# Kernel optimization log

Hardware: AMD Instinct MI355X
Metric: run time of the kernel (lower is better)

The kernel has to match this reference:

```python
import jax, jax.numpy as jnp
import numpy as np

D_MODEL = 1024
H = 16
D_K = D_MODEL // H  # 64
RANK = 5
ALPHA = 1.0


def _lora_linear(x, W, b, dW, dB):
    # merged weight: W + alpha * dB @ dW  (shape [out, in]); F.linear -> x @ W_merged.T + b
    Wm = W + ALPHA * (dB @ dW)
    return x @ Wm.T + b


def setup_inputs() -> dict:
    key = jax.random.key(0)
    ks = jax.random.split(key, 16)
    b_s, nq = 2, 2048
    s = 1.0 / np.sqrt(D_MODEL).astype(np.float32)
    inp = {
        "x": jax.random.normal(ks[0], (b_s, nq, D_MODEL), dtype=jnp.float32),
    }
    names = ["q", "k", "v", "o"]
    i = 1
    for n in names:
        inp[f"{n}_w"] = jax.random.normal(ks[i], (D_MODEL, D_MODEL), dtype=jnp.float32) * s; i += 1
        inp[f"{n}_b"] = jnp.zeros((D_MODEL,), dtype=jnp.float32)
        inp[f"{n}_dw"] = jax.random.normal(ks[i], (RANK, D_MODEL), dtype=jnp.float32) * 0.01; i += 1
        inp[f"{n}_db"] = jax.random.normal(ks[i], (D_MODEL, RANK), dtype=jnp.float32) * 0.01; i += 1
    return inp


def reference(x, q_w, q_b, q_dw, q_db, k_w, k_b, k_dw, k_db,
              v_w, v_b, v_dw, v_db, o_w, o_b, o_dw, o_db):
    b_s, nq, _ = x.shape
    q = _lora_linear(x, q_w, q_b, q_dw, q_db).reshape(b_s, nq, H, D_K)
    k = _lora_linear(x, k_w, k_b, k_dw, k_db).reshape(b_s, nq, H, D_K)
    v = _lora_linear(x, v_w, v_b, v_dw, v_db).reshape(b_s, nq, H, D_K)
    # scores: [b, h, q, k]
    att = jnp.einsum("bqhd,bkhd->bhqk", q, k) / np.sqrt(D_K).astype(np.float32)
    att = jax.nn.softmax(att, axis=-1)
    out = jnp.einsum("bhqk,bkhd->bqhd", att, v).reshape(b_s, nq, H * D_K)
    out = _lora_linear(out, o_w, o_b, o_dw, o_db)
    return out
```

## Files before the change

### kernel.cpp

```cpp
#include <hip/hip_runtime.h>
#include <hip/hip_bf16.h>

#define NQ 2048
#define NB 2

typedef unsigned short u16;
typedef unsigned int u32;
typedef _Float16 f16;
typedef __attribute__((ext_vector_type(8))) _Float16 half8;
typedef __attribute__((ext_vector_type(2))) __fp16 fp16x2;
typedef __attribute__((ext_vector_type(4))) float f32x4;

#define MFMAH(A, B, C) __builtin_amdgcn_mfma_f32_16x16x32_f16(A, B, C, 0, 0, 0)

__device__ __forceinline__ u16 f2h(float x) {
    f16 h = (f16)x;
    return *(u16*)&h;
}
__device__ __forceinline__ u32 pk_h2(float a, float b) {
    union { fp16x2 v; u32 u; } c;
    c.v = __builtin_amdgcn_cvt_pkrtz(a, b);
    return c.u;
}
__device__ __forceinline__ void glds16(const u16* g, u16* l) {
    typedef const __attribute__((address_space(1))) u16 gu16;
    typedef __attribute__((address_space(3))) u16 lu16;
    __builtin_amdgcn_global_load_lds((gu16*)g, (lu16*)l, 16, 0, 0);
}

__global__ __launch_bounds__(256) void merge_w16(
    const float* __restrict__ w0, const float* __restrict__ dw0, const float* __restrict__ db0,
    const float* __restrict__ w1, const float* __restrict__ dw1, const float* __restrict__ db1,
    const float* __restrict__ w2, const float* __restrict__ dw2, const float* __restrict__ db2,
    const float* __restrict__ w3, const float* __restrict__ dw3, const float* __restrict__ db3,
    u16* __restrict__ Wf) {
    int idx = blockIdx.x * 256 + threadIdx.x;
    int row = idx >> 10, col = idx & 1023;
    int which = row >> 10, lr = row & 1023;
    const float* W  = (which == 0) ? w0  : (which == 1) ? w1  : (which == 2) ? w2  : w3;
    const float* dW = (which == 0) ? dw0 : (which == 1) ? dw1 : (which == 2) ? dw2 : dw3;
    const float* dB = (which == 0) ? db0 : (which == 1) ? db1 : (which == 2) ? db2 : db3;
    float acc = W[lr * 1024 + col];
#pragma unroll
    for (int r = 0; r < 5; ++r) acc += dB[lr * 5 + r] * dW[r * 1024 + col];
    if (which == 0) acc *= 0.125f;
    Wf[idx] = f2h(acc);
}

__global__ __launch_bounds__(256) void bias_pack(
    const float* __restrict__ b0, const float* __restrict__ b1,
    const float* __restrict__ b2, const float* __restrict__ b3,
    float* __restrict__ ball) {
    int t = blockIdx.x * 256 + threadIdx.x;
    int which = t >> 10;
    const float* B = (which == 0) ? b0 : (which == 1) ? b1 : (which == 2) ? b2 : b3;
    float v = B[t & 1023];
    if (which == 0) v *= 0.125f;
    ball[t] = v;
}

__global__ __launch_bounds__(256) void xcast(const float* __restrict__ x,
                                             u16* __restrict__ xf) {
    int i4 = (blockIdx.x * 256 + threadIdx.x) * 4;
    float4 v = *(const float4*)&x[i4];
    *(uint2*)&xf[i4] = make_uint2(pk_h2(v.x, v.y), pk_h2(v.z, v.w));
}

template <int TM>
__global__ __launch_bounds__(256) void gemm_f16(
    const u16* __restrict__ Af, const u16* __restrict__ Bf,
    const float* __restrict__ bias,
    float* __restrict__ Cf, u16* __restrict__ Cb, int ldc,
    u16* __restrict__ VtOut) {
    constexpr int MI = TM / 32;
    __shared__ u16 As[2][TM * 32];
    __shared__ u16 Bs[2][128 * 32];
    const int tid = threadIdx.x;
    const int wid = tid >> 6, lane = tid & 63;
    const int ln = lane & 15, quad = lane >> 4;
    const int bm = blockIdx.y * TM, bn = blockIdx.x * 128;
    const int wm = (wid >> 1) * (TM / 2), wn = (wid & 1) * 64;
    const int lrow = lane >> 2;
    const int lchunk = (lane & 3) * 8;

    f32x4 acc[MI][4];
#pragma unroll
    for (int i = 0; i < MI; ++i)
#pragma unroll
        for (int j = 0; j < 4; ++j) acc[i][j] = (f32x4){0.f, 0.f, 0.f, 0.f};

    for (int k0 = 0; k0 < 1024; k0 += 64) {
#pragma unroll
        for (int hf = 0; hf < 2; ++hf) {
#pragma unroll
            for (int p = 0; p < TM / 64; ++p) {
                int r = p * 64 + wid * 16;
                glds16(&Af[(bm + r + lrow) * 1024 + k0 + hf * 32 + lchunk],
                       &As[hf][r * 32]);
            }
#pragma unroll
            for (int p = 0; p < 2; ++p) {
                int r = p * 64 + wid * 16;
                glds16(&Bf[(bn + r + lrow) * 1024 + k0 + hf * 32 + lchunk],
                       &Bs[hf][r * 32]);
            }
        }
        asm volatile("s_waitcnt vmcnt(0)" ::: "memory");
        __syncthreads();

        half8 a[MI][2], b[4][2];
#pragma unroll
        for (int kc = 0; kc < 2; ++kc) {
#pragma unroll
            for (int j = 0; j < 4; ++j)
                b[j][kc] = *(const half8*)&Bs[kc][(wn + j * 16 + ln) * 32 + quad * 8];
#pragma unroll
            for (int i = 0; i < MI; ++i)
                a[i][kc] = *(const half8*)&As[kc][(wm + i * 16 + ln) * 32 + quad * 8];
        }
#pragma unroll
        for (int i = 0; i < MI; ++i)
#pragma unroll
            for (int j = 0; j < 4; ++j) {
                acc[i][j] = MFMAH(a[i][0], b[j][0], acc[i][j]);
                acc[i][j] = MFMAH(a[i][1], b[j][1], acc[i][j]);
            }
        __syncthreads();
    }

    if (VtOut && bn >= 2048) {
#pragma unroll
        for (int i = 0; i < MI; ++i)
#pragma unroll
            for (int j = 0; j < 4; ++j) {
                int col = bn + wn + j * 16 + ln;
                float bv = bias[col];
                int colV = col - 2048;
                int row0 = bm + wm + i * 16 + quad * 4;
                ushort4 pk = make_ushort4(f2h(acc[i][j][0] + bv), f2h(acc[i][j][1] + bv),
                                          f2h(acc[i][j][2] + bv), f2h(acc[i][j][3] + bv));
                *(ushort4*)&VtOut[colV * 4096 + row0] = pk;
            }
        return;
    }

#pragma unroll
    for (int i = 0; i < MI; ++i)
#pragma unroll
        for (int j = 0; j < 4; ++j) {
            int col = bn + wn + j * 16 + ln;
            float bv = bias[col];
#pragma unroll
            for (int r = 0; r < 4; ++r) {
                int row = bm + wm + i * 16 + quad * 4 + r;
                float v = acc[i][j][r] + bv;
                if (Cb) Cb[row * ldc + col] = f2h(v);
                else    Cf[row * ldc + col] = v;
            }
        }
}

__global__ __launch_bounds__(256) void flash_f16(
    const u16* __restrict__ QKV, const u16* __restrict__ Vt,
    u16* __restrict__ AO) {
    __shared__ u16 Ks[2][64 * 72];
    __shared__ u16 Vs[2][64 * 72];
    __shared__ u16 Ps[4][32 * 72];

    const int tid = threadIdx.x;
    const int wid = tid >> 6, lane = tid & 63;
    const int ln = lane & 15, quad = lane >> 4;
    const int qt = blockIdx.x, h = blockIdx.y, b = blockIdx.z;
    const int rowbase = b * NQ;
    const int col0 = h * 64;
    const int q0 = rowbase + qt * 128 + wid * 32;

    const half8 ones = {(f16)1, (f16)1, (f16)1, (f16)1,
                        (f16)1, (f16)1, (f16)1, (f16)1};

    half8 qf[2][2];
#pragma unroll
    for (int mi = 0; mi < 2; ++mi)
#pragma unroll
        for (int kc = 0; kc < 2; ++kc)
            qf[mi][kc] = *(const half8*)&QKV[(q0 + mi * 16 + ln) * 3072 + col0 +
                                             kc * 32 + quad * 8];

    f32x4 accO[4][2];
    f32x4 accS[2];
#pragma unroll
    for (int mi = 0; mi < 2; ++mi) {
        accS[mi] = (f32x4){0.f, 0.f, 0.f, 0.f};
#pragma unroll
        for (int a = 0; a < 4; ++a) accO[a][mi] = (f32x4){0.f, 0.f, 0.f, 0.f};
    }

    const int srow = tid >> 2;
    const int sc0 = (tid & 3) * 16;
    const int NT = NQ / 64;

    {
        const u16* kg = QKV + (rowbase + srow) * 3072 + 1024 + col0;
        const u16* vg = Vt + (col0 + srow) * 4096 + rowbase;
        *(uint4*)&Ks[0][srow * 72 + sc0]     = *(const uint4*)&kg[sc0];
        *(uint4*)&Ks[0][srow * 72 + sc0 + 8] = *(const uint4*)&kg[sc0 + 8];
        *(uint4*)&Vs[0][srow * 72 + sc0]     = *(const uint4*)&vg[sc0];
        *(uint4*)&Vs[0][srow * 72 + sc0 + 8] = *(const uint4*)&vg[sc0 + 8];
    }
    __syncthreads();

    for (int kt = 0; kt < NT; ++kt) {
        const int cur = kt & 1;
        uint4 nk0, nk1, nv0, nv1;
        if (kt + 1 < NT) {
            const u16* kg = QKV + (rowbase + (kt + 1) * 64 + srow) * 3072 + 1024 + col0;
            const u16* vg = Vt + (col0 + srow) * 4096 + rowbase + (kt + 1) * 64;
            nk0 = *(const uint4*)&kg[sc0];
            nk1 = *(const uint4*)&kg[sc0 + 8];
            nv0 = *(const uint4*)&vg[sc0];
            nv1 = *(const uint4*)&vg[sc0 + 8];
        }

        f32x4 s[4][2];
#pragma unroll
        for (int a = 0; a < 4; ++a) {
            half8 kf0 = *(const half8*)&Ks[cur][(a * 16 + ln) * 72 + quad * 8];
            half8 kf1 = *(const half8*)&Ks[cur][(a * 16 + ln) * 72 + 32 + quad * 8];
#pragma unroll
            for (int mi = 0; mi < 2; ++mi) {
                f32x4 t = (f32x4){0.f, 0.f, 0.f, 0.f};
                t = MFMAH(kf0, qf[mi][0], t);
                t = MFMAH(kf1, qf[mi][1], t);
                s[a][mi] = t;
            }
        }

#pragma unroll
        for (int mi = 0; mi < 2; ++mi)
#pragma unroll
            for (int a = 0; a < 4; ++a) {
                float p0 = __expf(s[a][mi][0]), p1 = __expf(s[a][mi][1]);
                float p2 = __expf(s[a][mi][2]), p3 = __expf(s[a][mi][3]);
                uint2 w = make_uint2(pk_h2(p0, p1), pk_h2(p2, p3));
                *(uint2*)&Ps[wid][(mi * 16 + ln) * 72 + a * 16 + quad * 4] = w;
            }

        asm volatile("s_waitcnt lgkmcnt(0)" ::: "memory");

        half8 pf[2][2];
#pragma unroll
        for (int mi = 0; mi < 2; ++mi)
#pragma unroll
            for (int kc = 0; kc < 2; ++kc) {
                pf[mi][kc] = *(const half8*)&Ps[wid][(mi * 16 + ln) * 72 +
                                                     kc * 32 + quad * 8];
                accS[mi] = MFMAH(ones, pf[mi][kc], accS[mi]);
            }

#pragma unroll
        for (int a = 0; a < 4; ++a) {
            half8 vf0 = *(const half8*)&Vs[cur][(a * 16 + ln) * 72 + quad * 8];
            half8 vf1 = *(const half8*)&Vs[cur][(a * 16 + ln) * 72 + 32 + quad * 8];
#pragma unroll
            for (int mi = 0; mi < 2; ++mi) {
                accO[a][mi] = MFMAH(vf0, pf[mi][0], accO[a][mi]);
                accO[a][mi] = MFMAH(vf1, pf[mi][1], accO[a][mi]);
            }
        }

        if (kt + 1 < NT) {
            const int nb = cur ^ 1;
            *(uint4*)&Ks[nb][srow * 72 + sc0]     = nk0;
            *(uint4*)&Ks[nb][srow * 72 + sc0 + 8] = nk1;
            *(uint4*)&Vs[nb][srow * 72 + sc0]     = nv0;
            *(uint4*)&Vs[nb][srow * 72 + sc0 + 8] = nv1;
        }
        __syncthreads();
    }

#pragma unroll
    for (int mi = 0; mi < 2; ++mi) {
        float inv = 1.f / accS[mi][0];
        int q = q0 + mi * 16 + ln;
#pragma unroll
        for (int a = 0; a < 4; ++a) {
            ushort4 pk = make_ushort4(f2h(accO[a][mi][0] * inv),
                                      f2h(accO[a][mi][1] * inv),
                                      f2h(accO[a][mi][2] * inv),
                                      f2h(accO[a][mi][3] * inv));
            *(ushort4*)&AO[q * 1024 + col0 + a * 16 + quad * 4] = pk;
        }
    }
}

extern "C" void kernel_launch(void* const* d_in, const int* in_sizes, int n_in,
                              void* d_out, int out_size, void* d_ws, size_t ws_size,
                              hipStream_t stream) {
    const float* x = (const float*)d_in[0];
    const float* w[4]  = {(const float*)d_in[1],  (const float*)d_in[5],
                          (const float*)d_in[9],  (const float*)d_in[13]};
    const float* bv[4] = {(const float*)d_in[2],  (const float*)d_in[6],
                          (const float*)d_in[10], (const float*)d_in[14]};
    const float* dw[4] = {(const float*)d_in[3],  (const float*)d_in[7],
                          (const float*)d_in[11], (const float*)d_in[15]};
    const float* db[4] = {(const float*)d_in[4],  (const float*)d_in[8],
                          (const float*)d_in[12], (const float*)d_in[16]};

    u16* p = (u16*)d_ws;
    u16* Wf  = p; p += 4096 * 1024;
    u16* xf  = p; p += 4096 * 1024;
    u16* QKV = p; p += 4096 * 3072;
    u16* Vt  = p; p += 1024 * 4096;
    float* ball = (float*)p;
    u16* AO = xf;

    merge_w16<<<16384, 256, 0, stream>>>(w[0], dw[0], db[0], w[1], dw[1], db[1],
                                         w[2], dw[2], db[2], w[3], dw[3], db[3], Wf);
    bias_pack<<<16, 256, 0, stream>>>(bv[0], bv[1], bv[2], bv[3], ball);
    xcast<<<4096, 256, 0, stream>>>(x, xf);

    gemm_f16<128><<<dim3(24, 32), 256, 0, stream>>>(xf, Wf, ball,
                                                    nullptr, QKV, 3072, Vt);

    flash_f16<<<dim3(NQ / 128, 16, NB), 256, 0, stream>>>(QKV, Vt, AO);

    gemm_f16<64><<<dim3(8, 64), 256, 0, stream>>>(AO, Wf + 3072 * 1024,
                                                  ball + 3072, (float*)d_out, nullptr, 1024,
                                                  nullptr);
}
```

Measured before the change: 237.1 us.

## Use direct global-to-LDS loads for K/V tiles and fold log2e into Q scale

The K and V tile staging in the flash kernel now uses global_load_lds to copy straight into shared memory, replacing the register round-trip. The smem layout changes from padded 72-stride rows to unpadded 32-wide halves, which may add bank conflicts on fragment reads. Separately, the Q scale now includes log2(e), so the softmax can use the hardware exp2 instead of __expf, saving a multiply per element.

```diff
diff --git a/kernel.cpp b/kernel.cpp
--- a/kernel.cpp
+++ b/kernel.cpp
@@ -22,11 +22,20 @@
     c.v = __builtin_amdgcn_cvt_pkrtz(a, b);
     return c.u;
 }
+__device__ __forceinline__ float fexp2(float x) {
+#if __has_builtin(__builtin_amdgcn_exp2f)
+    return __builtin_amdgcn_exp2f(x);
+#else
+    return exp2f(x);
+#endif
+}
 __device__ __forceinline__ void glds16(const u16* g, u16* l) {
     typedef const __attribute__((address_space(1))) u16 gu16;
     typedef __attribute__((address_space(3))) u16 lu16;
     __builtin_amdgcn_global_load_lds((gu16*)g, (lu16*)l, 16, 0, 0);
 }
+
+#define QSCALE 0.18033688011112042f
 
 __global__ __launch_bounds__(256) void merge_w16(
     const float* __restrict__ w0, const float* __restrict__ dw0, const float* __restrict__ db0,
@@ -43,7 +52,7 @@
     float acc = W[lr * 1024 + col];
 #pragma unroll
     for (int r = 0; r < 5; ++r) acc += dB[lr * 5 + r] * dW[r * 1024 + col];
-    if (which == 0) acc *= 0.125f;
+    if (which == 0) acc *= QSCALE;
     Wf[idx] = f2h(acc);
 }
 
@@ -55,7 +64,7 @@
     int which = t >> 10;
     const float* B = (which == 0) ? b0 : (which == 1) ? b1 : (which == 2) ? b2 : b3;
     float v = B[t & 1023];
-    if (which == 0) v *= 0.125f;
+    if (which == 0) v *= QSCALE;
     ball[t] = v;
 }
 
@@ -163,8 +172,8 @@
 __global__ __launch_bounds__(256) void flash_f16(
     const u16* __restrict__ QKV, const u16* __restrict__ Vt,
     u16* __restrict__ AO) {
-    __shared__ u16 Ks[2][64 * 72];
-    __shared__ u16 Vs[2][64 * 72];
+    __shared__ u16 Ks[2][2][64 * 32];
+    __shared__ u16 Vs[2][2][64 * 32];
     __shared__ u16 Ps[4][32 * 72];
 
     const int tid = threadIdx.x;
@@ -174,6 +183,8 @@
     const int rowbase = b * NQ;
     const int col0 = h * 64;
     const int q0 = rowbase + qt * 128 + wid * 32;
+    const int drow = lane >> 2;
+    const int dchunk = (lane & 3) * 8;
 
     const half8 ones = {(f16)1, (f16)1, (f16)1, (f16)1,
                         (f16)1, (f16)1, (f16)1, (f16)1};
@@ -195,37 +206,35 @@
         for (int a = 0; a < 4; ++a) accO[a][mi] = (f32x4){0.f, 0.f, 0.f, 0.f};
     }
 
-    const int srow = tid >> 2;
-    const int sc0 = (tid & 3) * 16;
     const int NT = NQ / 64;
 
-    {
-        const u16* kg = QKV + (rowbase + srow) * 3072 + 1024 + col0;
-        const u16* vg = Vt + (col0 + srow) * 4096 + rowbase;
-        *(uint4*)&Ks[0][srow * 72 + sc0]     = *(const uint4*)&kg[sc0];
-        *(uint4*)&Ks[0][srow * 72 + sc0 + 8] = *(const uint4*)&kg[sc0 + 8];
-        *(uint4*)&Vs[0][srow * 72 + sc0]     = *(const uint4*)&vg[sc0];
-        *(uint4*)&Vs[0][srow * 72 + sc0 + 8] = *(const uint4*)&vg[sc0 + 8];
-    }
+#define STAGE(buf, kt)                                                                 \
+    {                                                                                  \
+        int ktbase = rowbase + (kt) * 64;                                              \
+        _Pragma("unroll")                                                              \
+        for (int hf = 0; hf < 2; ++hf)                                                 \
+            glds16(&QKV[(ktbase + wid * 16 + drow) * 3072 + 1024 + col0 + hf * 32 +    \
+                        dchunk],                                                       \
+                   &Ks[buf][hf][wid * 16 * 32]);                                       \
+        _Pragma("unroll")                                                              \
+        for (int kh = 0; kh < 2; ++kh)                                                 \
+            glds16(&Vt[(col0 + wid * 16 + drow) * 4096 + ktbase + kh * 32 + dchunk],   \
+                   &Vs[buf][kh][wid * 16 * 32]);                                       \
+    }
+
+    STAGE(0, 0)
+    asm volatile("s_waitcnt vmcnt(0)" ::: "memory");
     __syncthreads();
 
     for (int kt = 0; kt < NT; ++kt) {
         const int cur = kt & 1;
-        uint4 nk0, nk1, nv0, nv1;
-        if (kt + 1 < NT) {
-            const u16* kg = QKV + (rowbase + (kt + 1) * 64 + srow) * 3072 + 1024 + col0;
-            const u16* vg = Vt + (col0 + srow) * 4096 + rowbase + (kt + 1) * 64;
-            nk0 = *(const uint4*)&kg[sc0];
-            nk1 = *(const uint4*)&kg[sc0 + 8];
-            nv0 = *(const uint4*)&vg[sc0];
-            nv1 = *(const uint4*)&vg[sc0 + 8];
-        }
+        if (kt + 1 < NT) STAGE(cur ^ 1, kt + 1)
 
         f32x4 s[4][2];
 #pragma unroll
         for (int a = 0; a < 4; ++a) {
-            half8 kf0 = *(const half8*)&Ks[cur][(a * 16 + ln) * 72 + quad * 8];
-            half8 kf1 = *(const half8*)&Ks[cur][(a * 16 + ln) * 72 + 32 + quad * 8];
+            half8 kf0 = *(const half8*)&Ks[cur][0][(a * 16 + ln) * 32 + quad * 8];
+            half8 kf1 = *(const half8*)&Ks[cur][1][(a * 16 + ln) * 32 + quad * 8];
 #pragma unroll
             for (int mi = 0; mi < 2; ++mi) {
                 f32x4 t = (f32x4){0.f, 0.f, 0.f, 0.f};
@@ -239,8 +248,8 @@
         for (int mi = 0; mi < 2; ++mi)
 #pragma unroll
             for (int a = 0; a < 4; ++a) {
-                float p0 = __expf(s[a][mi][0]), p1 = __expf(s[a][mi][1]);
-                float p2 = __expf(s[a][mi][2]), p3 = __expf(s[a][mi][3]);
+                float p0 = fexp2(s[a][mi][0]), p1 = fexp2(s[a][mi][1]);
+                float p2 = fexp2(s[a][mi][2]), p3 = fexp2(s[a][mi][3]);
                 uint2 w = make_uint2(pk_h2(p0, p1), pk_h2(p2, p3));
                 *(uint2*)&Ps[wid][(mi * 16 + ln) * 72 + a * 16 + quad * 4] = w;
             }
@@ -259,8 +268,8 @@
 
 #pragma unroll
         for (int a = 0; a < 4; ++a) {
-            half8 vf0 = *(const half8*)&Vs[cur][(a * 16 + ln) * 72 + quad * 8];
-            half8 vf1 = *(const half8*)&Vs[cur][(a * 16 + ln) * 72 + 32 + quad * 8];
+            half8 vf0 = *(const half8*)&Vs[cur][0][(a * 16 + ln) * 32 + quad * 8];
+            half8 vf1 = *(const half8*)&Vs[cur][1][(a * 16 + ln) * 32 + quad * 8];
 #pragma unroll
             for (int mi = 0; mi < 2; ++mi) {
                 accO[a][mi] = MFMAH(vf0, pf[mi][0], accO[a][mi]);
@@ -268,13 +277,7 @@
             }
         }
 
-        if (kt + 1 < NT) {
-            const int nb = cur ^ 1;
-            *(uint4*)&Ks[nb][srow * 72 + sc0]     = nk0;
-            *(uint4*)&Ks[nb][srow * 72 + sc0 + 8] = nk1;
-            *(uint4*)&Vs[nb][srow * 72 + sc0]     = nv0;
-            *(uint4*)&Vs[nb][srow * 72 + sc0 + 8] = nv1;
-        }
+        asm volatile("s_waitcnt vmcnt(0)" ::: "memory");
         __syncthreads();
     }
 
@@ -291,6 +294,7 @@
             *(ushort4*)&AO[q * 1024 + col0 + a * 16 + quad * 4] = pk;
         }
     }
+#undef STAGE
 }
 
 extern "C" void kernel_launch(void* const* d_in, const int* in_sizes, int n_in,
```

Measured after the change: 243.5 us. +2.7%, slower.
